# Optimization experiments

Measured on AMD Instinct MI355X. Metric: run time of the kernel, lower is better.

The kernel has to match this reference:

```python
import jax, jax.numpy as jnp
import numpy as np

N_Q_HEADS = 16
N_KV_HEADS = 4
HEAD_DIM = 128
SLIDING_WINDOW = 1024
ROPE_BASE = 1024


def _rope_tables(L, dim):
    # half-truncate RoPE: first dim//4 freqs geometric, next dim//4 zero
    freqs = (1.0 / ROPE_BASE) ** jnp.linspace(0.0, 1.0, num=dim // 4)
    freqs = jnp.concatenate([freqs, jnp.zeros(dim // 4, dtype=freqs.dtype)])
    theta = jnp.arange(L, dtype=jnp.float32)[:, None] * freqs[None, :]  # (L, dim/2)
    cos = jnp.cos(theta)[None, :, None, :]  # (1, L, 1, dim/2)
    sin = jnp.sin(theta)[None, :, None, :]
    return cos, sin


def _rotate(x, cos, sin):
    # x: (B, L, H, D)
    x1, x2 = jnp.split(x, 2, axis=-1)
    return jnp.concatenate([x1 * cos + x2 * sin, -x1 * sin + x2 * cos], axis=-1)


def setup_inputs() -> dict:
    key = jax.random.key(0)
    k1, k2, k3, k4 = jax.random.split(key, 4)
    B, L, D = 1, 2048, 2048
    qkv_dim = (N_Q_HEADS + 2 * N_KV_HEADS) * HEAD_DIM  # 3072
    return {
        "x": jax.random.normal(k1, (B, L, D), dtype=jnp.float32),
        "Wqkv": jax.random.normal(k2, (D, qkv_dim), dtype=jnp.float32) * (D ** -0.5),
        "Wo": jax.random.normal(k3, (N_Q_HEADS * HEAD_DIM, D), dtype=jnp.float32) * ((N_Q_HEADS * HEAD_DIM) ** -0.5),
        "s": jax.random.normal(k4, (1, N_Q_HEADS), dtype=jnp.float32) * 0.1,
    }


def reference(x, Wqkv, Wo, s):
    B, L, D = x.shape
    H, QM, hd = N_KV_HEADS, N_Q_HEADS // N_KV_HEADS, HEAD_DIM

    proj = x @ Wqkv  # (B, L, (Hq + 2*Hkv) * hd)
    q, k, v = jnp.split(proj, (N_Q_HEADS * hd, (N_Q_HEADS + N_KV_HEADS) * hd), axis=-1)

    cos, sin = _rope_tables(L, hd)
    q = _rotate(q.reshape(B, L, -1, hd), cos, sin).reshape(B, L, H, QM, hd)
    k = _rotate(k.reshape(B, L, H, hd), cos, sin)
    v = v.reshape(B, L, H, hd)

    sm_scale = 1.0 / jnp.sqrt(jnp.float32(hd))
    q_pos = jnp.arange(L)[None, :, None]
    k_pos = jnp.arange(L)[None, None, :]
    causal = q_pos >= k_pos                       # (1, L, L)
    window = q_pos < k_pos + SLIDING_WINDOW       # index % 2 == 0 -> window active
    mask = causal & window

    # (B, H, M, Lq, Lk) attention logits
    attn = jnp.einsum("bqhmd,bkhd->bhmqk", q, k) * sm_scale
    # NOTE: faithful to source: -inf placed WHERE mask is True
    attn = jnp.where(mask, -jnp.inf, attn)

    sink = jnp.broadcast_to(s.reshape(B, H, QM, 1, 1), (B, H, QM, L, 1))
    w = jax.nn.softmax(jnp.concatenate([attn, sink], axis=-1), axis=-1)[..., :-1]

    out = jnp.einsum("bhmqk,bkhd->bqhmd", w, v).reshape(B, L, -1)
    return out @ Wo
```

## Files before the change

kernel.cpp:

```cpp
#include <hip/hip_runtime.h>
#include <hip/hip_bf16.h>
#include <math.h>

typedef __bf16 bf16;
typedef __bf16 bf16x8 __attribute__((ext_vector_type(8)));
typedef __bf16 bf16x4v __attribute__((ext_vector_type(4)));
typedef short s16x4 __attribute__((ext_vector_type(4)));
typedef float f32x4 __attribute__((ext_vector_type(4)));

#define GLD16(gp, lp) __builtin_amdgcn_global_load_lds( \
    (__attribute__((address_space(1))) void*)(void*)(gp), \
    (__attribute__((address_space(3))) void*)(lp), 16, 0, 0)

#define L_SEQ 2048
#define D_MODEL 2048
#define QKV_N 3072
#define HD 128
#define QSCALE 0.1275310242959836f
#define LOG2E 1.4426950408889634f

__global__ __launch_bounds__(256) void prep(const float* __restrict__ x,
                                            const float* __restrict__ Wqkv,
                                            const float* __restrict__ Wo,
                                            bf16* __restrict__ xb,
                                            bf16* __restrict__ wqkvT,
                                            bf16* __restrict__ woT) {
    __shared__ float tile[32][33];
    int bid = blockIdx.x;
    if (bid < 4096) {
        int idx = (bid * 256 + threadIdx.x) * 4;
        float4 f = *(const float4*)(x + idx);
        bf16x4v o;
        o.x = (bf16)f.x; o.y = (bf16)f.y; o.z = (bf16)f.z; o.w = (bf16)f.w;
        *(bf16x4v*)(xb + idx) = o;
        return;
    }
    bid -= 4096;
    const float* src; bf16* dst; long ld_s, ld_d; int bx, by;
    if (bid < 6144) { bx = bid % 96; by = bid / 96; src = Wqkv; dst = wqkvT; ld_s = QKV_N; ld_d = D_MODEL; }
    else { bid -= 6144; bx = bid & 63; by = bid >> 6; src = Wo; dst = woT; ld_s = D_MODEL; ld_d = D_MODEL; }
    const int tx = threadIdx.x & 31, ty = threadIdx.x >> 5;
    const long c = bx * 32 + tx, r0 = by * 32;
#pragma unroll
    for (int i = 0; i < 4; ++i)
        tile[ty + i * 8][tx] = src[(r0 + ty + i * 8) * ld_s + c];
    __syncthreads();
    const long c0 = bx * 32;
#pragma unroll
    for (int i = 0; i < 4; ++i)
        dst[(c0 + ty + i * 8) * ld_d + r0 + tx] = (bf16)tile[tx][ty + i * 8];
}

#define GEMM64_BODY(KDIM)                                                        \
    __shared__ __align__(16) bf16 As[64 * 32];                                   \
    __shared__ __align__(16) bf16 Bs[128 * 32];                                  \
    const int tid = threadIdx.x;                                                 \
    const int wid = tid >> 6, lane = tid & 63;                                   \
    const int quad = lane >> 4, l15 = lane & 15;                                 \
    const long m0 = (long)blockIdx.y * 64, n0 = (long)blockIdx.x * 128;          \
    const int srowA = wid * 16 + (lane >> 2);                                    \
    const int srowB = wid * 32 + (lane >> 2);                                    \
    const int scol = ((lane & 3) ^ ((lane >> 3) & 3)) * 8;                       \
    f32x4 acc[8];                                                                \
    _Pragma("unroll")                                                            \
    for (int j = 0; j < 8; ++j) acc[j] = (f32x4){0.f, 0.f, 0.f, 0.f};            \
    const bf16* Ap  = A  + (m0 + srowA) * KDIM + scol;                           \
    const bf16* Bp  = Bt + (n0 + srowB) * KDIM + scol;                           \
    const bf16* Bp2 = Bp + (long)16 * KDIM;                                      \
    bf16* lA  = &As[(wid * 16) * 32];                                            \
    bf16* lB  = &Bs[(wid * 32) * 32];                                            \
    bf16* lB2 = &Bs[(wid * 32 + 16) * 32];                                       \
    const int rsw = ((l15 >> 1) & 3);                                            \
    for (int k0 = 0; k0 < KDIM; k0 += 32) {                                      \
        GLD16(Ap + k0, lA);                                                      \
        GLD16(Bp + k0, lB);                                                      \
        GLD16(Bp2 + k0, lB2);                                                    \
        __syncthreads();                                                         \
        bf16x8 af = *(const bf16x8*)&As[(wid * 16 + l15) * 32 + (quad ^ rsw) * 8]; \
        bf16x8 bfr[8];                                                           \
        _Pragma("unroll")                                                        \
        for (int j = 0; j < 8; ++j)                                              \
            bfr[j] = *(const bf16x8*)&Bs[(j * 16 + l15) * 32 + (quad ^ rsw) * 8]; \
        _Pragma("unroll")                                                        \
        for (int j = 0; j < 8; ++j)                                              \
            acc[j] = __builtin_amdgcn_mfma_f32_16x16x32_bf16(af, bfr[j], acc[j], 0, 0, 0); \
        __syncthreads();                                                         \
    }

__global__ __launch_bounds__(256) void gemm_qkv(const bf16* __restrict__ A,
                                                const bf16* __restrict__ Bt,
                                                bf16* __restrict__ Qb,
                                                bf16* __restrict__ Kb,
                                                bf16* __restrict__ Vtb) {
    const int head = blockIdx.x;
    GEMM64_BODY(D_MODEL)

    if (head < 20) {
        const float sc = head < 16 ? QSCALE : 1.0f;
        bf16* dst = head < 16 ? Qb + (long)head * L_SEQ * HD
                              : Kb + (long)(head - 16) * L_SEQ * HD;
#pragma unroll
        for (int jj = 0; jj < 2; ++jj) {
            const int d0 = jj * 16 + l15;
            const float freq = exp2f((float)d0 * (-10.0f / 31.0f));
#pragma unroll
            for (int r = 0; r < 4; ++r) {
                const long row = m0 + wid * 16 + quad * 4 + r;
                float sn, cs;
                sincosf((float)row * freq, &sn, &cs);
                const float x1 = acc[jj][r], x2 = acc[jj + 4][r];
                dst[row * HD + d0]      = (bf16)((x1 * cs + x2 * sn) * sc);
                dst[row * HD + d0 + 64] = (bf16)((x2 * cs - x1 * sn) * sc);
            }
        }
#pragma unroll
        for (int jj = 2; jj < 4; ++jj) {
            const int d0 = jj * 16 + l15;
#pragma unroll
            for (int r = 0; r < 4; ++r) {
                const long row = m0 + wid * 16 + quad * 4 + r;
                dst[row * HD + d0]      = (bf16)(acc[jj][r] * sc);
                dst[row * HD + d0 + 64] = (bf16)(acc[jj + 4][r] * sc);
            }
        }
    } else {
        bf16* dst = Vtb + (long)(head - 20) * HD * L_SEQ;
        const long m = m0 + wid * 16 + quad * 4;
#pragma unroll
        for (int j = 0; j < 8; ++j) {
            const int d = j * 16 + l15;
            bf16x4v vv;
#pragma unroll
            for (int r = 0; r < 4; ++r) vv[r] = (bf16)acc[j][r];
            *(bf16x4v*)(dst + (long)d * L_SEQ + m) = vv;
        }
    }
}

__global__ __launch_bounds__(256) void gemm_out(const bf16* __restrict__ A,
                                                const bf16* __restrict__ Bt,
                                                float* __restrict__ C) {
    GEMM64_BODY(D_MODEL)
#pragma unroll
    for (int j = 0; j < 8; ++j) {
        const long m = m0 + wid * 16 + quad * 4;
        const long n = n0 + j * 16 + l15;
#pragma unroll
        for (int r = 0; r < 4; ++r)
            C[(m + r) * (long)D_MODEL + n] = acc[j][r];
    }
}

__global__ __launch_bounds__(256, 2) void attn_p(const bf16* __restrict__ Qb,
                                                 const bf16* __restrict__ Kb,
                                                 const bf16* __restrict__ Vtb,
                                                 bf16* __restrict__ Opart,
                                                 float* __restrict__ lpart) {
    __shared__ __align__(1024) char smem[65536];

    const int bid = blockIdx.x;
    int t, hq, half;
    if (bid < 256) { t = bid >> 5; hq = (bid & 31) >> 1; half = bid & 1; }
    else { int b2 = bid - 256; t = 8 + (b2 >> 5); hq = (b2 & 31) >> 1; half = b2 & 1; }
    const int h = hq >> 2;
    const int q0 = t * 128;
    const int tid = threadIdx.x;
    const int w = tid >> 6;
    const int lane = tid & 63;
    const int quad = lane >> 4, l15 = lane & 15;

    const bf16* Qg = Qb + (long)hq * L_SEQ * HD;
    const bf16* Kg = Kb + (long)h * L_SEQ * HD;
    const bf16* Vg = Vtb + (long)h * HD * L_SEQ;

    bf16x8 qb[2][4];
#pragma unroll
    for (int rf = 0; rf < 2; ++rf)
#pragma unroll
        for (int kkd = 0; kkd < 4; ++kkd)
            qb[rf][kkd] = *(const bf16x8*)(Qg + (long)(q0 + w * 32 + rf * 16 + l15) * HD
                                              + kkd * 32 + quad * 8);

    f32x4 oaccT[2][8];
#pragma unroll
    for (int rf = 0; rf < 2; ++rf)
#pragma unroll
        for (int j = 0; j < 8; ++j) oaccT[rf][j] = (f32x4){0.f, 0.f, 0.f, 0.f};
    float lacc[2] = {0.f, 0.f};

    const int locnt = (2 * t - 14 > 0) ? (2 * t - 14) : 0;
    const int n = locnt + 32 - 2 * t;
    const int cnt = n >> 1;

    auto ktile = [&](int idx) {
        const int i = 2 * idx + half;
        return (i < locnt) ? i : (2 * t + (i - locnt));
    };

    auto stage = [&](int idx, int buf) {
        const int k0 = ktile(idx) * 64;
        bf16* Ksb  = (bf16*)(smem + buf * 32768);
        bf16* Vtsb = (bf16*)(smem + buf * 32768 + 16384);
#pragma unroll
        for (int ii = 0; ii < 4; ++ii) {
            int rowb = w * 16 + ii * 4;
            int row = rowb + quad;
            GLD16(Kg + (long)(k0 + row) * HD + ((l15 ^ (row & 7)) * 8), &Ksb[rowb * 128]);
        }
#pragma unroll
        for (int ii = 0; ii < 4; ++ii) {
            int rowb = w * 32 + ii * 8;
            int row = rowb + (lane >> 3);
            GLD16(Vg + (long)row * L_SEQ + k0 + (((lane & 7) ^ (row & 7)) * 8), &Vtsb[rowb * 64]);
        }
    };

    stage(0, 0);

    for (int it = 0; it < cnt; ++it) {
        __syncthreads();
        if (it + 1 < cnt) stage(it + 1, (it + 1) & 1);

        const int kt = ktile(it);
        const int k0 = kt * 64;
        const bf16* Ks  = (const bf16*)(smem + (it & 1) * 32768);
        const bf16* Vts = (const bf16*)(smem + (it & 1) * 32768 + 16384);

        f32x4 sacc[2][4];
#pragma unroll
        for (int kb = 0; kb < 4; ++kb) {
            bf16x8 ka[4];
#pragma unroll
            for (int kkd = 0; kkd < 4; ++kkd)
                ka[kkd] = *(const bf16x8*)&Ks[(kb * 16 + l15) * 128 +
                                              (((kkd * 4 + quad) ^ (l15 & 7)) * 8)];
#pragma unroll
            for (int rf = 0; rf < 2; ++rf) {
                f32x4 acc = (f32x4){0.f, 0.f, 0.f, 0.f};
#pragma unroll
                for (int kkd = 0; kkd < 4; ++kkd)
                    acc = __builtin_amdgcn_mfma_f32_16x16x32_bf16(ka[kkd], qb[rf][kkd], acc, 0, 0, 0);
                sacc[rf][kb] = acc;
            }
        }

        const bool bnd = (kt == 2 * t) || (kt == 2 * t + 1) ||
                         (kt == 2 * t - 15) || (kt == 2 * t - 16);
        s16x4 pb[2][4];
#pragma unroll
        for (int rf = 0; rf < 2; ++rf) {
            const int qq = q0 + w * 32 + rf * 16 + l15;
#pragma unroll
            for (int kb = 0; kb < 4; ++kb) {
#pragma unroll
                for (int r = 0; r < 4; ++r) {
                    float v = sacc[rf][kb][r];
                    if (bnd) {
                        const int kk = k0 + kb * 16 + quad * 4 + r;
                        if (!((kk > qq) || (kk <= qq - 1024))) v = -1e30f;
                    }
                    const float p = exp2f(v);
                    lacc[rf] += p;
                    bf16 hp = (bf16)p;
                    pb[rf][kb][r] = __builtin_bit_cast(short, hp);
                }
            }
        }

#pragma unroll
        for (int j = 0; j < 8; ++j) {
            const int drow = j * 16 + l15;
#pragma unroll
            for (int kq = 0; kq < 4; ++kq) {
                const int pc = ((kq * 2 + (quad >> 1)) ^ (l15 & 7));
                s16x4 va = *(const s16x4*)((const char*)&Vts[drow * 64] + pc * 16 + (quad & 1) * 8);
#pragma unroll
                for (int rf = 0; rf < 2; ++rf)
                    oaccT[rf][j] = __builtin_amdgcn_mfma_f32_16x16x16bf16_1k(
                        va, pb[rf][kq], oaccT[rf][j], 0, 0, 0);
            }
        }
    }

#pragma unroll
    for (int rf = 0; rf < 2; ++rf) {
        lacc[rf] += __shfl_xor(lacc[rf], 16, 64);
        lacc[rf] += __shfl_xor(lacc[rf], 32, 64);
    }

    bf16* Od = Opart + (long)bid * 16384;
#pragma unroll
    for (int rf = 0; rf < 2; ++rf) {
        const int ql = w * 32 + rf * 16 + l15;
#pragma unroll
        for (int j = 0; j < 8; ++j) {
            bf16x4v ov;
#pragma unroll
            for (int r = 0; r < 4; ++r) ov[r] = (bf16)oaccT[rf][j][r];
            *(bf16x4v*)(Od + ql * 128 + j * 16 + quad * 4) = ov;
        }
        if (quad == 0) lpart[bid * 128 + ql] = lacc[rf];
    }
}

__global__ __launch_bounds__(256) void attn_combine(const bf16* __restrict__ Opart,
                                                    const float* __restrict__ lpart,
                                                    const float* __restrict__ sink,
                                                    bf16* __restrict__ attnb) {
    const int job = blockIdx.x >> 3, sub = blockIdx.x & 7;
    const int t = job >> 4, hq = job & 15;
    const int bid0 = (t < 8) ? (t * 32 + hq * 2) : (256 + (t - 8) * 32 + hq * 2);
    const int bid1 = bid0 + 1;
    const int e = sub * 2048 + threadIdx.x * 8;
    const int q = e >> 7, d0 = e & 127;
    bf16x8 o0 = *(const bf16x8*)(Opart + (long)bid0 * 16384 + q * 128 + d0);
    bf16x8 o1 = *(const bf16x8*)(Opart + (long)bid1 * 16384 + q * 128 + d0);
    const float l = lpart[bid0 * 128 + q] + lpart[bid1 * 128 + q] +
                    exp2f(sink[hq] * LOG2E);
    const float inv = 1.0f / l;
    bf16x8 ov;
#pragma unroll
    for (int r = 0; r < 8; ++r)
        ov[r] = (bf16)(((float)o0[r] + (float)o1[r]) * inv);
    *(bf16x8*)(attnb + (long)(t * 128 + q) * D_MODEL + hq * 128 + d0) = ov;
}

extern "C" void kernel_launch(void* const* d_in, const int* in_sizes, int n_in,
                              void* d_out, int out_size, void* d_ws, size_t ws_size,
                              hipStream_t stream) {
    (void)in_sizes; (void)n_in; (void)out_size; (void)ws_size;
    const float* x    = (const float*)d_in[0];
    const float* Wqkv = (const float*)d_in[1];
    const float* Wo   = (const float*)d_in[2];
    const float* s    = (const float*)d_in[3];
    float* out = (float*)d_out;

    char* ws = (char*)d_ws;
    bf16* xb    = (bf16*)ws;
    bf16* wqkvT = (bf16*)(ws + 8388608);
    bf16* Qb    = (bf16*)(ws + 20971520);
    bf16* Kb    = (bf16*)(ws + 29360128);
    bf16* Vtb   = (bf16*)(ws + 31457280);
    bf16* woT   = (bf16*)(ws + 33554432);
    bf16* attnb = (bf16*)(ws + 41943040);
    bf16* Opart = (bf16*)ws;
    float* lpart = (float*)(ws + 16777216);

    prep<<<14336, 256, 0, stream>>>(x, Wqkv, Wo, xb, wqkvT, woT);

    gemm_qkv<<<dim3(QKV_N / 128, L_SEQ / 64), 256, 0, stream>>>(
        xb, wqkvT, Qb, Kb, Vtb);

    attn_p<<<512, 256, 0, stream>>>(Qb, Kb, Vtb, Opart, lpart);

    attn_combine<<<2048, 256, 0, stream>>>(Opart, lpart, s, attnb);

    gemm_out<<<dim3(D_MODEL / 128, L_SEQ / 64), 256, 0, stream>>>(
        attnb, woT, out);
}
```

Baseline: 224.7 us.

## Enlarge GEMM tiles to 128x256 with double-buffered LDS staging

Both projection GEMMs move from 64x128 block tiles to 128x256 tiles on a 2x2 wave layout, each wave holding a 4x8 grid of MFMA accumulators. The K loop now double-buffers the LDS tiles so the next slice's global-to-LDS loads are issued while the current slice is being multiplied, which also drops one barrier per iteration. The larger tiles raise operand reuse per LDS read and cut global traffic. The cost is far fewer blocks (192 for QKV, 128 for the output GEMM), which may leave many of the 256 CUs idle, plus higher register pressure under launch_bounds(256,1).

```diff
diff --git a/kernel.cpp b/kernel.cpp
--- a/kernel.cpp
+++ b/kernel.cpp
@@ -51,50 +51,64 @@
         dst[(c0 + ty + i * 8) * ld_d + r0 + tx] = (bf16)tile[tx][ty + i * 8];
 }
 
-#define GEMM64_BODY(KDIM)                                                        \
-    __shared__ __align__(16) bf16 As[64 * 32];                                   \
-    __shared__ __align__(16) bf16 Bs[128 * 32];                                  \
+#define GEMM256_BODY(KDIM)                                                       \
+    __shared__ __align__(16) bf16 As[2][128 * 32];                               \
+    __shared__ __align__(16) bf16 Bs[2][256 * 32];                               \
     const int tid = threadIdx.x;                                                 \
     const int wid = tid >> 6, lane = tid & 63;                                   \
     const int quad = lane >> 4, l15 = lane & 15;                                 \
-    const long m0 = (long)blockIdx.y * 64, n0 = (long)blockIdx.x * 128;          \
-    const int srowA = wid * 16 + (lane >> 2);                                    \
-    const int srowB = wid * 32 + (lane >> 2);                                    \
+    const int wm = wid & 1, wn = wid >> 1;                                       \
+    const long m0 = (long)blockIdx.y * 128, n0 = (long)blockIdx.x * 256;         \
+    const int srowA = wid * 32 + (lane >> 2);                                    \
+    const int srowB = wid * 64 + (lane >> 2);                                    \
     const int scol = ((lane & 3) ^ ((lane >> 3) & 3)) * 8;                       \
-    f32x4 acc[8];                                                                \
+    f32x4 acc[4][8];                                                             \
     _Pragma("unroll")                                                            \
-    for (int j = 0; j < 8; ++j) acc[j] = (f32x4){0.f, 0.f, 0.f, 0.f};            \
-    const bf16* Ap  = A  + (m0 + srowA) * KDIM + scol;                           \
-    const bf16* Bp  = Bt + (n0 + srowB) * KDIM + scol;                           \
-    const bf16* Bp2 = Bp + (long)16 * KDIM;                                      \
-    bf16* lA  = &As[(wid * 16) * 32];                                            \
-    bf16* lB  = &Bs[(wid * 32) * 32];                                            \
-    bf16* lB2 = &Bs[(wid * 32 + 16) * 32];                                       \
+    for (int i = 0; i < 4; ++i)                                                  \
+        _Pragma("unroll")                                                        \
+        for (int j = 0; j < 8; ++j) acc[i][j] = (f32x4){0.f, 0.f, 0.f, 0.f};     \
+    const bf16* ApA  = A  + (m0 + srowA) * KDIM + scol;                          \
+    const bf16* ApA2 = ApA + (long)16 * KDIM;                                    \
+    const bf16* BpB0 = Bt + (n0 + srowB) * KDIM + scol;                          \
+    const bf16* BpB1 = BpB0 + (long)16 * KDIM;                                   \
+    const bf16* BpB2 = BpB0 + (long)32 * KDIM;                                   \
+    const bf16* BpB3 = BpB0 + (long)48 * KDIM;                                   \
     const int rsw = ((l15 >> 1) & 3);                                            \
+    auto stage = [&](int k0, int buf) {                                          \
+        GLD16(ApA  + k0, &As[buf][(wid * 32) * 32]);                             \
+        GLD16(ApA2 + k0, &As[buf][(wid * 32 + 16) * 32]);                        \
+        GLD16(BpB0 + k0, &Bs[buf][(wid * 64) * 32]);                             \
+        GLD16(BpB1 + k0, &Bs[buf][(wid * 64 + 16) * 32]);                        \
+        GLD16(BpB2 + k0, &Bs[buf][(wid * 64 + 32) * 32]);                        \
+        GLD16(BpB3 + k0, &Bs[buf][(wid * 64 + 48) * 32]);                        \
+    };                                                                           \
+    stage(0, 0);                                                                 \
     for (int k0 = 0; k0 < KDIM; k0 += 32) {                                      \
-        GLD16(Ap + k0, lA);                                                      \
-        GLD16(Bp + k0, lB);                                                      \
-        GLD16(Bp2 + k0, lB2);                                                    \
         __syncthreads();                                                         \
-        bf16x8 af = *(const bf16x8*)&As[(wid * 16 + l15) * 32 + (quad ^ rsw) * 8]; \
-        bf16x8 bfr[8];                                                           \
+        if (k0 + 32 < KDIM) stage(k0 + 32, ((k0 >> 5) + 1) & 1);                 \
+        const int buf = (k0 >> 5) & 1;                                           \
+        bf16x8 af[4], bfr[8];                                                    \
+        _Pragma("unroll")                                                        \
+        for (int i = 0; i < 4; ++i)                                              \
+            af[i] = *(const bf16x8*)&As[buf][(wm * 64 + i * 16 + l15) * 32 + (quad ^ rsw) * 8]; \
         _Pragma("unroll")                                                        \
         for (int j = 0; j < 8; ++j)                                              \
-            bfr[j] = *(const bf16x8*)&Bs[(j * 16 + l15) * 32 + (quad ^ rsw) * 8]; \
+            bfr[j] = *(const bf16x8*)&Bs[buf][(wn * 128 + j * 16 + l15) * 32 + (quad ^ rsw) * 8]; \
         _Pragma("unroll")                                                        \
-        for (int j = 0; j < 8; ++j)                                              \
-            acc[j] = __builtin_amdgcn_mfma_f32_16x16x32_bf16(af, bfr[j], acc[j], 0, 0, 0); \
-        __syncthreads();                                                         \
-    }
-
-__global__ __launch_bounds__(256) void gemm_qkv(const bf16* __restrict__ A,
-                                                const bf16* __restrict__ Bt,
-                                                bf16* __restrict__ Qb,
-                                                bf16* __restrict__ Kb,
-                                                bf16* __restrict__ Vtb) {
-    const int head = blockIdx.x;
-    GEMM64_BODY(D_MODEL)
-
+        for (int i = 0; i < 4; ++i)                                              \
+            _Pragma("unroll")                                                    \
+            for (int j = 0; j < 8; ++j)                                          \
+                acc[i][j] = __builtin_amdgcn_mfma_f32_16x16x32_bf16(af[i], bfr[j], acc[i][j], 0, 0, 0); \
+    }
+
+__global__ __launch_bounds__(256, 1) void gemm_qkv(const bf16* __restrict__ A,
+                                                   const bf16* __restrict__ Bt,
+                                                   bf16* __restrict__ Qb,
+                                                   bf16* __restrict__ Kb,
+                                                   bf16* __restrict__ Vtb) {
+    GEMM256_BODY(D_MODEL)
+
+    const int head = blockIdx.x * 2 + wn;
     if (head < 20) {
         const float sc = head < 16 ? QSCALE : 1.0f;
         bf16* dst = head < 16 ? Qb + (long)head * L_SEQ * HD
@@ -104,50 +118,60 @@
             const int d0 = jj * 16 + l15;
             const float freq = exp2f((float)d0 * (-10.0f / 31.0f));
 #pragma unroll
-            for (int r = 0; r < 4; ++r) {
-                const long row = m0 + wid * 16 + quad * 4 + r;
-                float sn, cs;
-                sincosf((float)row * freq, &sn, &cs);
-                const float x1 = acc[jj][r], x2 = acc[jj + 4][r];
-                dst[row * HD + d0]      = (bf16)((x1 * cs + x2 * sn) * sc);
-                dst[row * HD + d0 + 64] = (bf16)((x2 * cs - x1 * sn) * sc);
-            }
+            for (int i = 0; i < 4; ++i)
+#pragma unroll
+                for (int r = 0; r < 4; ++r) {
+                    const long row = m0 + wm * 64 + i * 16 + quad * 4 + r;
+                    float sn, cs;
+                    sincosf((float)row * freq, &sn, &cs);
+                    const float x1 = acc[i][jj][r], x2 = acc[i][jj + 4][r];
+                    dst[row * HD + d0]      = (bf16)((x1 * cs + x2 * sn) * sc);
+                    dst[row * HD + d0 + 64] = (bf16)((x2 * cs - x1 * sn) * sc);
+                }
         }
 #pragma unroll
         for (int jj = 2; jj < 4; ++jj) {
             const int d0 = jj * 16 + l15;
 #pragma unroll
-            for (int r = 0; r < 4; ++r) {
-                const long row = m0 + wid * 16 + quad * 4 + r;
-                dst[row * HD + d0]      = (bf16)(acc[jj][r] * sc);
-                dst[row * HD + d0 + 64] = (bf16)(acc[jj + 4][r] * sc);
-            }
+            for (int i = 0; i < 4; ++i)
+#pragma unroll
+                for (int r = 0; r < 4; ++r) {
+                    const long row = m0 + wm * 64 + i * 16 + quad * 4 + r;
+                    dst[row * HD + d0]      = (bf16)(acc[i][jj][r] * sc);
+                    dst[row * HD + d0 + 64] = (bf16)(acc[i][jj + 4][r] * sc);
+                }
         }
     } else {
         bf16* dst = Vtb + (long)(head - 20) * HD * L_SEQ;
-        const long m = m0 + wid * 16 + quad * 4;
+#pragma unroll
+        for (int i = 0; i < 4; ++i) {
+            const long m = m0 + wm * 64 + i * 16 + quad * 4;
+#pragma unroll
+            for (int j = 0; j < 8; ++j) {
+                const int d = j * 16 + l15;
+                bf16x4v vv;
+#pragma unroll
+                for (int r = 0; r < 4; ++r) vv[r] = (bf16)acc[i][j][r];
+                *(bf16x4v*)(dst + (long)d * L_SEQ + m) = vv;
+            }
+        }
+    }
+}
+
+__global__ __launch_bounds__(256, 1) void gemm_out(const bf16* __restrict__ A,
+                                                   const bf16* __restrict__ Bt,
+                                                   float* __restrict__ C) {
+    GEMM256_BODY(D_MODEL)
+#pragma unroll
+    for (int i = 0; i < 4; ++i) {
+        const long m = m0 + wm * 64 + i * 16 + quad * 4;
 #pragma unroll
         for (int j = 0; j < 8; ++j) {
-            const int d = j * 16 + l15;
-            bf16x4v vv;
-#pragma unroll
-            for (int r = 0; r < 4; ++r) vv[r] = (bf16)acc[j][r];
-            *(bf16x4v*)(dst + (long)d * L_SEQ + m) = vv;
-        }
-    }
-}
-
-__global__ __launch_bounds__(256) void gemm_out(const bf16* __restrict__ A,
-                                                const bf16* __restrict__ Bt,
-                                                float* __restrict__ C) {
-    GEMM64_BODY(D_MODEL)
-#pragma unroll
-    for (int j = 0; j < 8; ++j) {
-        const long m = m0 + wid * 16 + quad * 4;
-        const long n = n0 + j * 16 + l15;
-#pragma unroll
-        for (int r = 0; r < 4; ++r)
-            C[(m + r) * (long)D_MODEL + n] = acc[j][r];
+            const long n = n0 + wn * 128 + j * 16 + l15;
+#pragma unroll
+            for (int r = 0; r < 4; ++r)
+                C[(m + r) * (long)D_MODEL + n] = acc[i][j][r];
+        }
     }
 }
 
@@ -348,13 +372,13 @@
 
     prep<<<14336, 256, 0, stream>>>(x, Wqkv, Wo, xb, wqkvT, woT);
 
-    gemm_qkv<<<dim3(QKV_N / 128, L_SEQ / 64), 256, 0, stream>>>(
+    gemm_qkv<<<dim3(QKV_N / 256, L_SEQ / 128), 256, 0, stream>>>(
         xb, wqkvT, Qb, Kb, Vtb);
 
     attn_p<<<512, 256, 0, stream>>>(Qb, Kb, Vtb, Opart, lpart);
 
     attn_combine<<<2048, 256, 0, stream>>>(Opart, lpart, s, attnb);
 
-    gemm_out<<<dim3(D_MODEL / 128, L_SEQ / 64), 256, 0, stream>>>(
+    gemm_out<<<dim3(D_MODEL / 256, L_SEQ / 128), 256, 0, stream>>>(
         attnb, woT, out);
 }
```

Measured after the change: 270.5 us. 1.2x slower.

## Use 128x128 double-buffered tiles with 2x2 warp layout in QKV GEMM

Applied to the files above, without the earlier changes.

The QKV projection GEMM moves from a 64x128 tile, where each warp owns 16 rows, to a 128x128 tile with a 2x2 warp grid. Each warp now computes a 64x64 sub-tile from 4 A and 4 B fragments, which raises MFMA work per LDS read. Shared memory is double-buffered so the next K-slice is loaded asynchronously while the current one is computed, leaving one barrier per iteration. The RoPE and V-transpose epilogues are remapped to the new accumulator layout. In exchange the grid shrinks to 384 blocks and register and LDS use go up, which may lower occupancy and wave fill on the GPU. The gemm_out kernel keeps the old body inlined.

```diff
diff --git a/kernel.cpp b/kernel.cpp
--- a/kernel.cpp
+++ b/kernel.cpp
@@ -51,88 +51,96 @@
         dst[(c0 + ty + i * 8) * ld_d + r0 + tx] = (bf16)tile[tx][ty + i * 8];
 }
 
-#define GEMM64_BODY(KDIM)                                                        \
-    __shared__ __align__(16) bf16 As[64 * 32];                                   \
-    __shared__ __align__(16) bf16 Bs[128 * 32];                                  \
-    const int tid = threadIdx.x;                                                 \
-    const int wid = tid >> 6, lane = tid & 63;                                   \
-    const int quad = lane >> 4, l15 = lane & 15;                                 \
-    const long m0 = (long)blockIdx.y * 64, n0 = (long)blockIdx.x * 128;          \
-    const int srowA = wid * 16 + (lane >> 2);                                    \
-    const int srowB = wid * 32 + (lane >> 2);                                    \
-    const int scol = ((lane & 3) ^ ((lane >> 3) & 3)) * 8;                       \
-    f32x4 acc[8];                                                                \
-    _Pragma("unroll")                                                            \
-    for (int j = 0; j < 8; ++j) acc[j] = (f32x4){0.f, 0.f, 0.f, 0.f};            \
-    const bf16* Ap  = A  + (m0 + srowA) * KDIM + scol;                           \
-    const bf16* Bp  = Bt + (n0 + srowB) * KDIM + scol;                           \
-    const bf16* Bp2 = Bp + (long)16 * KDIM;                                      \
-    bf16* lA  = &As[(wid * 16) * 32];                                            \
-    bf16* lB  = &Bs[(wid * 32) * 32];                                            \
-    bf16* lB2 = &Bs[(wid * 32 + 16) * 32];                                       \
-    const int rsw = ((l15 >> 1) & 3);                                            \
-    for (int k0 = 0; k0 < KDIM; k0 += 32) {                                      \
-        GLD16(Ap + k0, lA);                                                      \
-        GLD16(Bp + k0, lB);                                                      \
-        GLD16(Bp2 + k0, lB2);                                                    \
-        __syncthreads();                                                         \
-        bf16x8 af = *(const bf16x8*)&As[(wid * 16 + l15) * 32 + (quad ^ rsw) * 8]; \
-        bf16x8 bfr[8];                                                           \
-        _Pragma("unroll")                                                        \
-        for (int j = 0; j < 8; ++j)                                              \
-            bfr[j] = *(const bf16x8*)&Bs[(j * 16 + l15) * 32 + (quad ^ rsw) * 8]; \
-        _Pragma("unroll")                                                        \
-        for (int j = 0; j < 8; ++j)                                              \
-            acc[j] = __builtin_amdgcn_mfma_f32_16x16x32_bf16(af, bfr[j], acc[j], 0, 0, 0); \
-        __syncthreads();                                                         \
-    }
-
-__global__ __launch_bounds__(256) void gemm_qkv(const bf16* __restrict__ A,
-                                                const bf16* __restrict__ Bt,
-                                                bf16* __restrict__ Qb,
-                                                bf16* __restrict__ Kb,
-                                                bf16* __restrict__ Vtb) {
+__global__ __launch_bounds__(256, 2) void gemm_qkv(const bf16* __restrict__ A,
+                                                   const bf16* __restrict__ Bt,
+                                                   bf16* __restrict__ Qb,
+                                                   bf16* __restrict__ Kb,
+                                                   bf16* __restrict__ Vtb) {
+    constexpr int KDIM = D_MODEL;
+    __shared__ __align__(16) bf16 As[2][128 * 32];
+    __shared__ __align__(16) bf16 Bs[2][128 * 32];
+    const int tid = threadIdx.x;
+    const int wid = tid >> 6, lane = tid & 63;
+    const int quad = lane >> 4, l15 = lane & 15;
+    const int wm = wid & 1, wn = wid >> 1;
     const int head = blockIdx.x;
-    GEMM64_BODY(D_MODEL)
+    const long m0 = (long)blockIdx.y * 128, n0 = (long)head * 128;
+
+    const int srow = wid * 32 + (lane >> 2);
+    const int scol = ((lane & 3) ^ ((lane >> 3) & 3)) * 8;
+
+    f32x4 acc[4][4];
+#pragma unroll
+    for (int i = 0; i < 4; ++i)
+#pragma unroll
+        for (int j = 0; j < 4; ++j) acc[i][j] = (f32x4){0.f, 0.f, 0.f, 0.f};
+
+    const bf16* ApA  = A  + (m0 + srow) * KDIM + scol;
+    const bf16* ApA2 = ApA + (long)16 * KDIM;
+    const bf16* BpB  = Bt + (n0 + srow) * KDIM + scol;
+    const bf16* BpB2 = BpB + (long)16 * KDIM;
+    const int rsw = ((l15 >> 1) & 3);
+
+    auto stage = [&](int k0, int buf) {
+        GLD16(ApA  + k0, &As[buf][(wid * 32) * 32]);
+        GLD16(ApA2 + k0, &As[buf][(wid * 32 + 16) * 32]);
+        GLD16(BpB  + k0, &Bs[buf][(wid * 32) * 32]);
+        GLD16(BpB2 + k0, &Bs[buf][(wid * 32 + 16) * 32]);
+    };
+    stage(0, 0);
+
+    for (int k0 = 0; k0 < KDIM; k0 += 32) {
+        __syncthreads();
+        if (k0 + 32 < KDIM) stage(k0 + 32, ((k0 >> 5) + 1) & 1);
+        const int buf = (k0 >> 5) & 1;
+        bf16x8 af[4], bfr[4];
+#pragma unroll
+        for (int i = 0; i < 4; ++i)
+            af[i] = *(const bf16x8*)&As[buf][(wm * 64 + i * 16 + l15) * 32 + (quad ^ rsw) * 8];
+#pragma unroll
+        for (int j = 0; j < 4; ++j)
+            bfr[j] = *(const bf16x8*)&Bs[buf][(j * 32 + wn * 16 + l15) * 32 + (quad ^ rsw) * 8];
+#pragma unroll
+        for (int i = 0; i < 4; ++i)
+#pragma unroll
+            for (int j = 0; j < 4; ++j)
+                acc[i][j] = __builtin_amdgcn_mfma_f32_16x16x32_bf16(af[i], bfr[j], acc[i][j], 0, 0, 0);
+    }
 
     if (head < 20) {
         const float sc = head < 16 ? QSCALE : 1.0f;
         bf16* dst = head < 16 ? Qb + (long)head * L_SEQ * HD
                               : Kb + (long)(head - 16) * L_SEQ * HD;
-#pragma unroll
-        for (int jj = 0; jj < 2; ++jj) {
-            const int d0 = jj * 16 + l15;
-            const float freq = exp2f((float)d0 * (-10.0f / 31.0f));
+        const int d0 = wn * 16 + l15;
+        const float freq = exp2f((float)d0 * (-10.0f / 31.0f));
+        const int d1 = 32 + wn * 16 + l15;
+#pragma unroll
+        for (int i = 0; i < 4; ++i)
 #pragma unroll
             for (int r = 0; r < 4; ++r) {
-                const long row = m0 + wid * 16 + quad * 4 + r;
+                const long row = m0 + wm * 64 + i * 16 + quad * 4 + r;
                 float sn, cs;
                 sincosf((float)row * freq, &sn, &cs);
-                const float x1 = acc[jj][r], x2 = acc[jj + 4][r];
-                dst[row * HD + d0]      = (bf16)((x1 * cs + x2 * sn) * sc);
-                dst[row * HD + d0 + 64] = (bf16)((x2 * cs - x1 * sn) * sc);
+                const float x1 = acc[i][0][r], x2 = acc[i][2][r];
+                bf16* p = dst + row * HD;
+                p[d0]      = (bf16)((x1 * cs + x2 * sn) * sc);
+                p[d0 + 64] = (bf16)((x2 * cs - x1 * sn) * sc);
+                p[d1]      = (bf16)(acc[i][1][r] * sc);
+                p[d1 + 64] = (bf16)(acc[i][3][r] * sc);
             }
-        }
-#pragma unroll
-        for (int jj = 2; jj < 4; ++jj) {
-            const int d0 = jj * 16 + l15;
-#pragma unroll
-            for (int r = 0; r < 4; ++r) {
-                const long row = m0 + wid * 16 + quad * 4 + r;
-                dst[row * HD + d0]      = (bf16)(acc[jj][r] * sc);
-                dst[row * HD + d0 + 64] = (bf16)(acc[jj + 4][r] * sc);
-            }
-        }
     } else {
         bf16* dst = Vtb + (long)(head - 20) * HD * L_SEQ;
-        const long m = m0 + wid * 16 + quad * 4;
-#pragma unroll
-        for (int j = 0; j < 8; ++j) {
-            const int d = j * 16 + l15;
-            bf16x4v vv;
-#pragma unroll
-            for (int r = 0; r < 4; ++r) vv[r] = (bf16)acc[j][r];
-            *(bf16x4v*)(dst + (long)d * L_SEQ + m) = vv;
+#pragma unroll
+        for (int i = 0; i < 4; ++i) {
+            const long m = m0 + wm * 64 + i * 16 + quad * 4;
+#pragma unroll
+            for (int j = 0; j < 4; ++j) {
+                const int d = j * 32 + wn * 16 + l15;
+                bf16x4v vv;
+#pragma unroll
+                for (int r = 0; r < 4; ++r) vv[r] = (bf16)acc[i][j][r];
+                *(bf16x4v*)(dst + (long)d * L_SEQ + m) = vv;
+            }
         }
     }
 }
@@ -140,7 +148,41 @@
 __global__ __launch_bounds__(256) void gemm_out(const bf16* __restrict__ A,
                                                 const bf16* __restrict__ Bt,
                                                 float* __restrict__ C) {
-    GEMM64_BODY(D_MODEL)
+    constexpr int KDIM = D_MODEL;
+    __shared__ __align__(16) bf16 As[64 * 32];
+    __shared__ __align__(16) bf16 Bs[128 * 32];
+    const int tid = threadIdx.x;
+    const int wid = tid >> 6, lane = tid & 63;
+    const int quad = lane >> 4, l15 = lane & 15;
+    const long m0 = (long)blockIdx.y * 64, n0 = (long)blockIdx.x * 128;
+    const int srowA = wid * 16 + (lane >> 2);
+    const int srowB = wid * 32 + (lane >> 2);
+    const int scol = ((lane & 3) ^ ((lane >> 3) & 3)) * 8;
+    f32x4 acc[8];
+#pragma unroll
+    for (int j = 0; j < 8; ++j) acc[j] = (f32x4){0.f, 0.f, 0.f, 0.f};
+    const bf16* Ap  = A  + (m0 + srowA) * KDIM + scol;
+    const bf16* Bp  = Bt + (n0 + srowB) * KDIM + scol;
+    const bf16* Bp2 = Bp + (long)16 * KDIM;
+    bf16* lA  = &As[(wid * 16) * 32];
+    bf16* lB  = &Bs[(wid * 32) * 32];
+    bf16* lB2 = &Bs[(wid * 32 + 16) * 32];
+    const int rsw = ((l15 >> 1) & 3);
+    for (int k0 = 0; k0 < KDIM; k0 += 32) {
+        GLD16(Ap + k0, lA);
+        GLD16(Bp + k0, lB);
+        GLD16(Bp2 + k0, lB2);
+        __syncthreads();
+        bf16x8 af = *(const bf16x8*)&As[(wid * 16 + l15) * 32 + (quad ^ rsw) * 8];
+        bf16x8 bfr[8];
+#pragma unroll
+        for (int j = 0; j < 8; ++j)
+            bfr[j] = *(const bf16x8*)&Bs[(j * 16 + l15) * 32 + (quad ^ rsw) * 8];
+#pragma unroll
+        for (int j = 0; j < 8; ++j)
+            acc[j] = __builtin_amdgcn_mfma_f32_16x16x32_bf16(af, bfr[j], acc[j], 0, 0, 0);
+        __syncthreads();
+    }
 #pragma unroll
     for (int j = 0; j < 8; ++j) {
         const long m = m0 + wid * 16 + quad * 4;
@@ -348,7 +390,7 @@
 
     prep<<<14336, 256, 0, stream>>>(x, Wqkv, Wo, xb, wqkvT, woT);
 
-    gemm_qkv<<<dim3(QKV_N / 128, L_SEQ / 64), 256, 0, stream>>>(
+    gemm_qkv<<<dim3(QKV_N / 128, L_SEQ / 128), 256, 0, stream>>>(
         xb, wqkvT, Qb, Kb, Vtb);
 
     attn_p<<<512, 256, 0, stream>>>(Qb, Kb, Vtb, Opart, lpart);
```

After: 230.1 us. +2.4%, slower.
